# Kernel tuning notes

Hardware: AMD Instinct MI355X
Metric: run time of the kernel (lower is better)

The kernel has to match this reference:

```python
import jax, jax.numpy as jnp
import numpy as np

IOU_THRESHOLD = 0.3
NUM_CLASSES = 80
BG_IDX = NUM_CLASSES
EPS = 1e-09
TOPK_FALLBACK = 3


def _make_boxes(key, shape, img=640.0):
    # shape = (..., 4); produce valid x1y1x2y2 boxes
    k1, k2 = jax.random.split(key)
    xy = jax.random.uniform(k1, shape[:-1] + (2,)) * img
    wh = jax.random.uniform(k2, shape[:-1] + (2,)) * 128.0 + 8.0
    return jnp.concatenate([xy - wh / 2, xy + wh / 2], axis=-1).astype(jnp.float32)


def setup_inputs() -> dict:
    key = jax.random.key(0)
    ks = jax.random.split(key, 6)
    bs, A, G = 16, 33600, 64
    pd_scores = jax.random.normal(ks[0], (bs, A, NUM_CLASSES), dtype=jnp.float32)
    pd_bboxes = _make_boxes(ks[1], (bs, A, 4))
    anc_points = jax.random.uniform(ks[2], (A, 2), dtype=jnp.float32) * 640.0
    gt_labels = jax.random.randint(ks[3], (bs, G, 1), 0, NUM_CLASSES).astype(jnp.int64)
    gt_bboxes = _make_boxes(ks[4], (bs, G, 4))
    mask_gt = jax.random.randint(ks[5], (bs, G, 1), 0, 2).astype(jnp.int32)
    return {"pd_scores": pd_scores, "pd_bboxes": pd_bboxes, "anc_points": anc_points,
            "gt_labels": gt_labels, "gt_bboxes": gt_bboxes, "mask_gt": mask_gt}


def _pairwise_iou(gt, pd):
    # gt: (bs, G, 4), pd: (bs, A, 4) -> (bs, G, A)
    b1 = gt[:, :, None, :]   # (bs, G, 1, 4)
    b2 = pd[:, None, :, :]   # (bs, 1, A, 4)
    iw = jnp.clip(jnp.minimum(b1[..., 2], b2[..., 2]) - jnp.maximum(b1[..., 0], b2[..., 0]), 0)
    ih = jnp.clip(jnp.minimum(b1[..., 3], b2[..., 3]) - jnp.maximum(b1[..., 1], b2[..., 1]), 0)
    inter = iw * ih
    a1 = (b1[..., 2] - b1[..., 0]) * (b1[..., 3] - b1[..., 1])
    a2 = (b2[..., 2] - b2[..., 0]) * (b2[..., 3] - b2[..., 1])
    return inter / (a1 + a2 - inter + EPS)


def reference(pd_scores, pd_bboxes, anc_points, gt_labels, gt_bboxes, mask_gt):
    bs, G, _ = gt_bboxes.shape
    A = anc_points.shape[0]
    valid = mask_gt[..., 0].astype(bool)                      # (bs, G)

    # IoU matrix; rows of invalid GTs are zero (original writes only valid rows)
    overlaps = _pairwise_iou(gt_bboxes, pd_bboxes) * valid[:, :, None]  # (bs, G, A)

    pos_mask = (overlaps > IOU_THRESHOLD) & valid[:, :, None]
    fg_any = pos_mask.any(axis=(1, 2))                        # (bs,)

    # Per-batch top-k fallback when a batch has zero positives but has valid GTs
    masked = jnp.where(valid[:, :, None], overlaps, -jnp.inf)
    top_vals, _ = jax.lax.top_k(masked.reshape(bs, G * A), TOPK_FALLBACK)
    min_iou = top_vals[:, -1]                                 # (bs,)
    fb_pos = (overlaps >= min_iou[:, None, None]) & valid[:, :, None]
    has_valid = valid.any(axis=1)
    need_fb = (~fg_any) & has_valid
    pos_mask = jnp.where(need_fb[:, None, None], fb_pos, pos_mask)
    fg_mask = pos_mask.any(axis=1)                            # (bs, A)

    # Assignment: argmax over GT axis (first-max, like torch.argmax)
    target_gt_idx = jnp.argmax(overlaps, axis=1)              # (bs, A)

    batch_idx = jnp.arange(bs)[:, None]
    valid_assign = valid[batch_idx, target_gt_idx]            # (bs, A)
    mask = fg_mask & valid_assign

    labels_g = gt_labels[..., 0][batch_idx, target_gt_idx]    # (bs, A)
    target_labels = jnp.where(mask, labels_g, BG_IDX).astype(jnp.int64)
    boxes_g = gt_bboxes[batch_idx, target_gt_idx]             # (bs, A, 4)
    target_bboxes = boxes_g * mask[..., None].astype(boxes_g.dtype)
    # one_hot zeroes out-of-range class indices, matching the explicit range check
    target_scores = jax.nn.one_hot(labels_g, NUM_CLASSES, dtype=jnp.float32) * mask[..., None]

    return (target_labels, target_bboxes, target_scores, fg_mask, target_gt_idx)
```

## Files before the change

kernel.cpp:

```cpp
#include <hip/hip_runtime.h>
#include <math.h>

#define NC 80
constexpr int BS  = 16;
constexpr int NA  = 33600;
constexpr int NG  = 64;
constexpr int TPB = 256;
constexpr int NBLK = (NA + TPB - 1) / TPB;
constexpr int NW   = TPB / 64;

__device__ __forceinline__ void ins3(float v, float& t0, float& t1, float& t2) {
  t2 = fmaxf(t2, fminf(v, t1));
  t1 = fmaxf(t1, fminf(v, t0));
  t0 = fmaxf(t0, v);
}

__device__ __forceinline__ void wave_top3(float& t0, float& t1, float& t2) {
  #pragma unroll
  for (int off = 32; off > 0; off >>= 1) {
    float u0 = __shfl_xor(t0, off, 64);
    float u1 = __shfl_xor(t1, off, 64);
    float u2 = __shfl_xor(t2, off, 64);
    ins3(u0, t0, t1, t2);
    ins3(u1, t0, t1, t2);
    ins3(u2, t0, t1, t2);
  }
}

__global__ __launch_bounds__(TPB) void p1_kernel(
    const float4* __restrict__ pd, const float4* __restrict__ gt,
    const int* __restrict__ glab, const int* __restrict__ gmask,
    float* __restrict__ outL, float4* __restrict__ outB,
    float* __restrict__ outS, float* __restrict__ outF,
    float* __restrict__ outI, float* __restrict__ blockTop)
{
  #pragma clang fp contract(off)
  const int b   = blockIdx.y;
  const int tid = threadIdx.x;

  __shared__ float4 sbox[NG];
  __shared__ float  sarea[NG];
  __shared__ int    slab[NG];
  __shared__ int    svalid[NG];

  const int a0  = blockIdx.x * TPB;
  const int a   = a0 + tid;
  const bool inb = a < NA;

  float4 p = make_float4(0.f, 0.f, 0.f, 0.f);
  if (inb) p = pd[(long)b * NA + a];

  if (tid < NG) {
    int v = gmask[b * NG + tid];
    float4 g = gt[b * NG + tid];
    if (!v) g = make_float4(0.f, 0.f, 0.f, 0.f);
    sbox[tid]   = g;
    sarea[tid]  = (g.z - g.x) * (g.w - g.y);
    slab[tid]   = glab[b * NG + tid];
    svalid[tid] = v;
  }
  __syncthreads();

  const int nA = min(TPB, NA - a0);
  float4* s4 = (float4*)(outS + ((long)b * NA + a0) * NC);
  const int cnt4 = nA * (NC / 4);
  for (int i = tid; i < cnt4; i += TPB) s4[i] = make_float4(0.f, 0.f, 0.f, 0.f);

  float t0 = -INFINITY, t1 = -INFINITY, t2 = -INFINITY;
  float best = -1.f;
  int   bidx = 0;
  bool  maskv = false;
  int   blab  = 0;

  if (inb) {
    const float a2 = (p.z - p.x) * (p.w - p.y);
    #pragma unroll 8
    for (int g = 0; g < NG; ++g) {
      float4 gb = sbox[g];
      float iw = fminf(gb.z, p.z) - fmaxf(gb.x, p.x);
      float ih = fminf(gb.w, p.w) - fmaxf(gb.y, p.y);
      iw = fmaxf(iw, 0.f);
      ih = fmaxf(ih, 0.f);
      float inter = iw * ih;
      float den   = sarea[g] + a2 - inter + 1e-9f;
      float iou   = inter / den;
      bidx = (iou > best) ? g : bidx;
      best = fmaxf(best, iou);
      ins3(iou, t0, t1, t2);
    }
    bool fg = best > 0.3f;
    maskv = fg && (svalid[bidx] != 0);
    blab  = slab[bidx];
    long ga = (long)b * NA + a;
    outL[ga] = maskv ? (float)blab : 80.f;
    float m = maskv ? 1.f : 0.f;
    float4 gb = sbox[bidx];
    outB[ga] = make_float4(gb.x * m, gb.y * m, gb.z * m, gb.w * m);
    outF[ga] = fg ? 1.f : 0.f;
    outI[ga] = (float)bidx;
  }

  wave_top3(t0, t1, t2);

  __syncthreads();

  const int lane = tid & 63, wid = tid >> 6;
  if (lane == 0) {
    float* bt = blockTop + (((long)b * NBLK + blockIdx.x) * NW + wid) * 3;
    bt[0] = t0; bt[1] = t1; bt[2] = t2;
  }

  if (inb && maskv) outS[((long)b * NA + a) * NC + blab] = 1.f;
}

__global__ __launch_bounds__(TPB) void p3_kernel(
    const float4* __restrict__ pd, const float4* __restrict__ gt,
    const int* __restrict__ glab, const int* __restrict__ gmask,
    const float* __restrict__ blockTop,
    float* __restrict__ outL, float4* __restrict__ outB,
    float* __restrict__ outS, float* __restrict__ outF)
{
  #pragma clang fp contract(off)
  const int b   = blockIdx.y;
  const int tid = threadIdx.x;

  __shared__ float  swt[NW][3];
  __shared__ float  sres;
  __shared__ int    sfb;
  __shared__ float4 sbox[NG];
  __shared__ float  sarea[NG];
  __shared__ int    slab[NG];
  __shared__ int    svalid[NG];

  int gv = (tid < NG) ? gmask[b * NG + tid] : 0;
  unsigned long long bal = __ballot(gv != 0);

  float t0 = -INFINITY, t1 = -INFINITY, t2 = -INFINITY;
  for (int i = tid; i < NBLK * NW; i += TPB) {
    const float* bt = blockTop + ((long)b * NBLK * NW + i) * 3;
    ins3(bt[0], t0, t1, t2);
    ins3(bt[1], t0, t1, t2);
    ins3(bt[2], t0, t1, t2);
  }
  wave_top3(t0, t1, t2);
  const int lane = tid & 63, wid = tid >> 6;
  if (lane == 0) { swt[wid][0] = t0; swt[wid][1] = t1; swt[wid][2] = t2; }
  __syncthreads();
  if (tid == 0) {
    float r0 = swt[0][0], r1 = swt[0][1], r2 = swt[0][2];
    #pragma unroll
    for (int w = 1; w < NW; ++w) {
      ins3(swt[w][0], r0, r1, r2);
      ins3(swt[w][1], r0, r1, r2);
      ins3(swt[w][2], r0, r1, r2);
    }
    sfb  = (!(r0 > 0.3f) && bal != 0ULL) ? 1 : 0;
    sres = r2;
  }
  if (tid < NG) {
    float4 g = gt[b * NG + tid];
    if (!gv) g = make_float4(0.f, 0.f, 0.f, 0.f);
    sbox[tid]   = g;
    sarea[tid]  = (g.z - g.x) * (g.w - g.y);
    slab[tid]   = glab[b * NG + tid];
    svalid[tid] = gv;
  }
  __syncthreads();
  if (sfb == 0) return;
  const float minio = sres;

  const int a = blockIdx.x * TPB + tid;
  if (a >= NA) return;

  float4 p  = pd[(long)b * NA + a];
  float  a2 = (p.z - p.x) * (p.w - p.y);
  float best = -1.f;
  int   bidx = 0;
  #pragma unroll 8
  for (int g = 0; g < NG; ++g) {
    float4 gb = sbox[g];
    float iw = fminf(gb.z, p.z) - fmaxf(gb.x, p.x);
    float ih = fminf(gb.w, p.w) - fmaxf(gb.y, p.y);
    iw = fmaxf(iw, 0.f);
    ih = fmaxf(ih, 0.f);
    float inter = iw * ih;
    float den   = sarea[g] + a2 - inter + 1e-9f;
    float iou   = inter / den;
    bidx = (iou > best) ? g : bidx;
    best = fmaxf(best, iou);
  }
  bool fg    = best >= minio;
  bool maskv = fg && (svalid[bidx] != 0);
  int  blab  = slab[bidx];
  long ga = (long)b * NA + a;
  outL[ga] = maskv ? (float)blab : 80.f;
  float m = maskv ? 1.f : 0.f;
  float4 gb = sbox[bidx];
  outB[ga] = make_float4(gb.x * m, gb.y * m, gb.z * m, gb.w * m);
  outF[ga] = fg ? 1.f : 0.f;
  if (maskv) outS[ga * NC + blab] = 1.f;
}

extern "C" void kernel_launch(void* const* d_in, const int* in_sizes, int n_in,
                              void* d_out, int out_size, void* d_ws, size_t ws_size,
                              hipStream_t stream) {
  const float4* pd    = (const float4*)d_in[1];
  const int*    glab  = (const int*)d_in[3];
  const float4* gt    = (const float4*)d_in[4];
  const int*    gmask = (const int*)d_in[5];

  float* outf = (float*)d_out;
  float*  outL = outf;
  float4* outB = (float4*)(outf + (long)BS * NA);
  float*  outS = outf + (long)BS * NA * 5;
  float*  outF = outf + (long)BS * NA * 5 + (long)BS * NA * NC;
  float*  outI = outF + (long)BS * NA;

  float* blockTop = (float*)d_ws;

  dim3 grid(NBLK, BS);
  p1_kernel<<<grid, TPB, 0, stream>>>(pd, gt, glab, gmask,
                                      outL, outB, outS, outF, outI, blockTop);
  p3_kernel<<<grid, TPB, 0, stream>>>(pd, gt, glab, gmask, blockTop,
                                      outL, outB, outS, outF);
}
```

Before: 298.6 us.

## Split score zero-fill into its own kernel and skip top-3 work when positives exist

The zeroing of the large target_scores buffer moves from p1 into a separate grid-stride fill kernel that runs first. p1 now stores a per-wave max IoU and only runs a second IoU pass with top-3 insertion when that wave has no positive. p3 first reduces the per-wave maxima and exits early when the batch already has positives, skipping the top-3 merge and GT loads. This removes the per-iteration top-3 cost and shuffle reductions in the common case. The cost is an extra kernel launch and a second IoU pass for waves with no positives.

New measurement: 317.6 us. 6.4% more time.

```diff
diff --git a/kernel.cpp b/kernel.cpp
--- a/kernel.cpp
+++ b/kernel.cpp
@@ -25,6 +25,14 @@
     ins3(u1, t0, t1, t2);
     ins3(u2, t0, t1, t2);
   }
+}
+
+__global__ __launch_bounds__(TPB) void fill_kernel(float4* __restrict__ s4, long n4)
+{
+  const long stride = (long)gridDim.x * TPB;
+  const float4 z = make_float4(0.f, 0.f, 0.f, 0.f);
+  for (long i = (long)blockIdx.x * TPB + threadIdx.x; i < n4; i += stride)
+    s4[i] = z;
 }
 
 __global__ __launch_bounds__(TPB) void p1_kernel(
@@ -61,19 +69,12 @@
   }
   __syncthreads();
 
-  const int nA = min(TPB, NA - a0);
-  float4* s4 = (float4*)(outS + ((long)b * NA + a0) * NC);
-  const int cnt4 = nA * (NC / 4);
-  for (int i = tid; i < cnt4; i += TPB) s4[i] = make_float4(0.f, 0.f, 0.f, 0.f);
-
-  float t0 = -INFINITY, t1 = -INFINITY, t2 = -INFINITY;
   float best = -1.f;
   int   bidx = 0;
-  bool  maskv = false;
-  int   blab  = 0;
+  float a2 = 0.f;
 
   if (inb) {
-    const float a2 = (p.z - p.x) * (p.w - p.y);
+    a2 = (p.z - p.x) * (p.w - p.y);
     #pragma unroll 8
     for (int g = 0; g < NG; ++g) {
       float4 gb = sbox[g];
@@ -86,11 +87,10 @@
       float iou   = inter / den;
       bidx = (iou > best) ? g : bidx;
       best = fmaxf(best, iou);
-      ins3(iou, t0, t1, t2);
     }
-    bool fg = best > 0.3f;
-    maskv = fg && (svalid[bidx] != 0);
-    blab  = slab[bidx];
+    bool fg    = best > 0.3f;
+    bool maskv = fg && (svalid[bidx] != 0);
+    int  blab  = slab[bidx];
     long ga = (long)b * NA + a;
     outL[ga] = maskv ? (float)blab : 80.f;
     float m = maskv ? 1.f : 0.f;
@@ -98,19 +98,36 @@
     outB[ga] = make_float4(gb.x * m, gb.y * m, gb.z * m, gb.w * m);
     outF[ga] = fg ? 1.f : 0.f;
     outI[ga] = (float)bidx;
-  }
-
-  wave_top3(t0, t1, t2);
-
-  __syncthreads();
-
-  const int lane = tid & 63, wid = tid >> 6;
-  if (lane == 0) {
-    float* bt = blockTop + (((long)b * NBLK + blockIdx.x) * NW + wid) * 3;
-    bt[0] = t0; bt[1] = t1; bt[2] = t2;
-  }
-
-  if (inb && maskv) outS[((long)b * NA + a) * NC + blab] = 1.f;
+    if (maskv) outS[ga * NC + blab] = 1.f;
+  }
+
+  float wmax = best;
+  #pragma unroll
+  for (int off = 32; off > 0; off >>= 1)
+    wmax = fmaxf(wmax, __shfl_xor(wmax, off, 64));
+
+  float* bt = blockTop + (((long)b * NBLK + blockIdx.x) * NW + (tid >> 6)) * 3;
+
+  if (wmax <= 0.3f) {
+    float t0 = -INFINITY, t1 = -INFINITY, t2 = -INFINITY;
+    if (inb) {
+      #pragma unroll 4
+      for (int g = 0; g < NG; ++g) {
+        float4 gb = sbox[g];
+        float iw = fminf(gb.z, p.z) - fmaxf(gb.x, p.x);
+        float ih = fminf(gb.w, p.w) - fmaxf(gb.y, p.y);
+        iw = fmaxf(iw, 0.f);
+        ih = fmaxf(ih, 0.f);
+        float inter = iw * ih;
+        float den   = sarea[g] + a2 - inter + 1e-9f;
+        float iou   = inter / den;
+        ins3(iou, t0, t1, t2);
+      }
+    }
+    wave_top3(t0, t1, t2);
+    if ((tid & 63) == 0) { bt[1] = t1; bt[2] = t2; }
+  }
+  if ((tid & 63) == 0) bt[0] = wmax;
 }
 
 __global__ __launch_bounds__(TPB) void p3_kernel(
@@ -124,6 +141,8 @@
   const int b   = blockIdx.y;
   const int tid = threadIdx.x;
 
+  __shared__ float  swm[NW];
+  __shared__ float  sM;
   __shared__ float  swt[NW][3];
   __shared__ float  sres;
   __shared__ int    sfb;
@@ -132,6 +151,24 @@
   __shared__ int    slab[NG];
   __shared__ int    svalid[NG];
 
+  float m = -INFINITY;
+  for (int i = tid; i < NBLK * NW; i += TPB)
+    m = fmaxf(m, blockTop[((long)b * NBLK * NW + i) * 3]);
+  #pragma unroll
+  for (int off = 32; off > 0; off >>= 1)
+    m = fmaxf(m, __shfl_xor(m, off, 64));
+  const int lane = tid & 63, wid = tid >> 6;
+  if (lane == 0) swm[wid] = m;
+  __syncthreads();
+  if (tid == 0) {
+    float r = swm[0];
+    #pragma unroll
+    for (int w = 1; w < NW; ++w) r = fmaxf(r, swm[w]);
+    sM = r;
+  }
+  __syncthreads();
+  if (sM > 0.3f) return;
+
   int gv = (tid < NG) ? gmask[b * NG + tid] : 0;
   unsigned long long bal = __ballot(gv != 0);
 
@@ -143,7 +180,6 @@
     ins3(bt[2], t0, t1, t2);
   }
   wave_top3(t0, t1, t2);
-  const int lane = tid & 63, wid = tid >> 6;
   if (lane == 0) { swt[wid][0] = t0; swt[wid][1] = t1; swt[wid][2] = t2; }
   __syncthreads();
   if (tid == 0) {
@@ -194,9 +230,9 @@
   int  blab  = slab[bidx];
   long ga = (long)b * NA + a;
   outL[ga] = maskv ? (float)blab : 80.f;
-  float m = maskv ? 1.f : 0.f;
+  float mm = maskv ? 1.f : 0.f;
   float4 gb = sbox[bidx];
-  outB[ga] = make_float4(gb.x * m, gb.y * m, gb.z * m, gb.w * m);
+  outB[ga] = make_float4(gb.x * mm, gb.y * mm, gb.z * mm, gb.w * mm);
   outF[ga] = fg ? 1.f : 0.f;
   if (maskv) outS[ga * NC + blab] = 1.f;
 }
@@ -218,9 +254,13 @@
 
   float* blockTop = (float*)d_ws;
 
+  const long n4 = (long)BS * NA * NC / 4;
+  fill_kernel<<<2048, TPB, 0, stream>>>((float4*)outS, n4);
+
   dim3 grid(NBLK, BS);
   p1_kernel<<<grid, TPB, 0, stream>>>(pd, gt, glab, gmask,
                                       outL, outB, outS, outF, outI, blockTop);
+
   p3_kernel<<<grid, TPB, 0, stream>>>(pd, gt, glab, gmask, blockTop,
                                       outL, outB, outS, outF);
 }
```
